# Kernel optimization log

Hardware: AMD Instinct MI355X
Metric: run time of the kernel (lower is better)

Reference implementation:

```python
import jax, jax.numpy as jnp
import numpy as np
import math

R, C, B, E, H, F = 64, 256, 1, 768, 12, 3072
D = E // H  # head dim = 64
EPS = 1e-6  # flax LayerNorm default


def _ln(x, s, b):
    mu = jnp.mean(x, axis=-1, keepdims=True)
    var = jnp.mean((x - mu) ** 2, axis=-1, keepdims=True)
    return (x - mu) * jax.lax.rsqrt(var + EPS) * s + b


def setup_inputs() -> dict:
    key = jax.random.key(0)
    ks = jax.random.split(key, 16)
    w = lambda k, sh: jax.random.normal(k, sh, jnp.float32) * 0.02
    z = lambda sh: jnp.zeros(sh, jnp.float32)
    return {
        "x": jax.random.normal(ks[0], (R, C, B, E), jnp.float32),
        "ln1_s": jnp.ones((E,), jnp.float32), "ln1_b": z((E,)),
        "r_wq": w(ks[1], (E, E)), "r_bq": z((E,)),
        "r_wk": w(ks[2], (E, E)), "r_bk": z((E,)),
        "r_wv": w(ks[3], (E, E)), "r_bv": z((E,)),
        "r_wo": w(ks[4], (E, E)), "r_bo": z((E,)),
        "ln2_s": jnp.ones((E,), jnp.float32), "ln2_b": z((E,)),
        "c_wq": w(ks[5], (E, E)), "c_bq": z((E,)),
        "c_wk": w(ks[6], (E, E)), "c_bk": z((E,)),
        "c_wv": w(ks[7], (E, E)), "c_bv": z((E,)),
        "c_wo": w(ks[8], (E, E)), "c_bo": z((E,)),
        "ln3_s": jnp.ones((E,), jnp.float32), "ln3_b": z((E,)),
        "f_w1": w(ks[9], (E, F)), "f_b1": z((F,)),
        "f_w2": w(ks[10], (F, E)), "f_b2": z((E,)),
    }


def reference(x, ln1_s, ln1_b, r_wq, r_bq, r_wk, r_bk, r_wv, r_bv, r_wo, r_bo,
              ln2_s, ln2_b, c_wq, c_bq, c_wk, c_bk, c_wv, c_bv, c_wo, c_bo,
              ln3_s, ln3_b, f_w1, f_b1, f_w2, f_b2):
    qkv = (R, C, B, H, D)
    # --- tied row self-attention (NOTE: original code has no residual adds) ---
    h = _ln(x, ln1_s, ln1_b)
    q = (h @ r_wq + r_bq).reshape(qkv) * (D ** -0.5 / math.sqrt(R))  # tied-row scaling
    k = (h @ r_wk + r_bk).reshape(qkv)
    v = (h @ r_wv + r_bv).reshape(qkv)
    aw = jnp.einsum('rinhd,rjnhd->hnij', q, k)  # single softmax tied across rows
    ap = jax.nn.softmax(aw, axis=-1)
    ctx = jnp.einsum('hnij,rjnhd->rinhd', ap, v).reshape(R, C, B, E)
    x = ctx @ r_wo + r_bo
    # --- column self-attention (per-column attention over rows) ---
    h = _ln(x, ln2_s, ln2_b)
    q = (h @ c_wq + c_bq).reshape(qkv) * (D ** -0.5)
    k = (h @ c_wk + c_bk).reshape(qkv)
    v = (h @ c_wv + c_bv).reshape(qkv)
    aw = jnp.einsum('icnhd,jcnhd->hcnij', q, k)
    ap = jax.nn.softmax(aw, axis=-1)
    ctx = jnp.einsum('hcnij,jcnhd->icnhd', ap, v).reshape(R, C, B, E)
    x = ctx @ c_wo + c_bo
    # --- FFN (gelu approximate=True matches flax default) ---
    h = _ln(x, ln3_s, ln3_b)
    return jax.nn.gelu(h @ f_w1 + f_b1) @ f_w2 + f_b2
```

## Files before the change

### kernel.cpp

```cpp
#include <hip/hip_runtime.h>
#include <hip/hip_bf16.h>
#include <stdint.h>
#include <stddef.h>

#define R_ 64
#define C_ 256
#define E_ 768
#define H_ 12
#define F_ 3072
#define D_ 64
#define NT_ (R_*C_)
#define HCRD_ ((size_t)H_*C_*R_*D_)

typedef float f32x4 __attribute__((ext_vector_type(4)));
typedef __bf16 bf16x8 __attribute__((ext_vector_type(8)));
typedef unsigned short us4 __attribute__((ext_vector_type(4)));
typedef unsigned short us8 __attribute__((ext_vector_type(8)));

typedef __attribute__((address_space(3))) uint32_t lds_u32;
typedef __attribute__((address_space(1))) uint32_t glb_u32;

__device__ __forceinline__ void gld16(const uint16_t* g, uint16_t* l) {
  __builtin_amdgcn_global_load_lds((const glb_u32*)g, (lds_u32*)l, 16, 0, 0);
}

__device__ __forceinline__ uint16_t f2b(float f) {
  __bf16 h = (__bf16)f;
  return *(uint16_t*)&h;
}

#define VM_WAIT6 { asm volatile("s_waitcnt vmcnt(6)" ::: "memory"); __builtin_amdgcn_sched_barrier(0); }
#define VM_WAIT4 { asm volatile("s_waitcnt vmcnt(4)" ::: "memory"); __builtin_amdgcn_sched_barrier(0); }
#define VM_WAIT0 { asm volatile("s_waitcnt vmcnt(0)" ::: "memory"); __builtin_amdgcn_sched_barrier(0); }
#define BARRIER  { __builtin_amdgcn_s_barrier(); __builtin_amdgcn_sched_barrier(0); }

enum { EP_F32B = 0, EP_GELU = 1, EP_AW = 2, EP_CTX = 3, EP_QKVROW = 4, EP_QKVCOL = 5 };

template<int EP, bool PERM>
__global__ __launch_bounds__(512, 2)
void gemm256(const uint16_t* __restrict__ A, const uint16_t* __restrict__ B,
             const float* __restrict__ bias, const float* __restrict__ biasK,
             const float* __restrict__ biasV, void* __restrict__ out,
             int N, int K, int lda, int ldb, float scale)
{
  __shared__ uint16_t lds[2][4][8192];
  const int tid  = threadIdx.x;
  const int wave = tid >> 6, lane = tid & 63;
  const int wm = wave >> 2, wn = wave & 3;
  const int lr = lane & 15, lq = lane >> 4;

  int lin = blockIdx.x + gridDim.x * blockIdx.y;
  const int q8 = (gridDim.x * gridDim.y) >> 3;
  const int wid = (lin & 7) * q8 + (lin >> 3);
  const int bx = wid % gridDim.x, by = wid / gridDim.x;
  const long bm = (long)by * 256, bn = (long)bx * 256;

  const int r0 = tid >> 2;
  const int csw = (((tid & 3) ^ ((r0 >> 1) & 3)) * 8);
  long am0 = bm + r0, am1 = bm + r0 + 128;
  if constexpr (PERM) {
    am0 = ((am0 & 63) << 8) | (am0 >> 6);
    am1 = ((am1 & 63) << 8) | (am1 >> 6);
  }
  const uint16_t* aR0 = A + am0 * (long)lda + csw;
  const uint16_t* aR1 = A + am1 * (long)lda + csw;
  const uint16_t* bR0 = B + (bn + r0) * (long)ldb + csw;
  const uint16_t* bR1 = B + (bn + r0 + 128) * (long)ldb + csw;

  auto stageH = [&](int s) {
    const int u = s >> 2, j = s & 3;
    const int kb = u * 64 + (j >> 1) * 32;
    uint16_t* d = &lds[u & 1][j][0];
    if (j & 1) { gld16(aR0 + kb, d + tid * 8); gld16(aR1 + kb, d + (tid + 512) * 8); }
    else       { gld16(bR0 + kb, d + tid * 8); gld16(bR1 + kb, d + (tid + 512) * 8); }
  };
  auto aoff = [&](int row) { return row * 32 + ((lq ^ ((row >> 1) & 3)) * 8); };

  f32x4 acc[8][4];
#pragma unroll
  for (int i = 0; i < 8; ++i)
#pragma unroll
    for (int j = 0; j < 4; ++j) acc[i][j] = (f32x4){0.f, 0.f, 0.f, 0.f};

  const int nt = K >> 6;
  stageH(0); stageH(1); stageH(2); stageH(3);
  VM_WAIT4;
  stageH(4); stageH(5); stageH(6);
  VM_WAIT6;
  BARRIER;

  for (int t = 0; t < nt; ++t) {
    const int buf = t & 1;
    const uint16_t* B0h = &lds[buf][0][0];
    const uint16_t* A0h = &lds[buf][1][0];
    const uint16_t* B1h = &lds[buf][2][0];
    const uint16_t* A1h = &lds[buf][3][0];
    const int s0 = 4 * t + 7;
    bf16x8 af[4], bf[4];

#pragma unroll
    for (int i = 0; i < 4; ++i) {
      bf[i] = *(const bf16x8*)&B0h[aoff(wn * 64 + i * 16 + lr)];
      af[i] = *(const bf16x8*)&A0h[aoff(wm * 128 + i * 16 + lr)];
    }
    if (s0 < 4 * nt) stageH(s0);
    BARRIER;
    __builtin_amdgcn_s_setprio(1);
#pragma unroll
    for (int mi = 0; mi < 4; ++mi)
#pragma unroll
      for (int ni = 0; ni < 4; ++ni)
        acc[mi][ni] = __builtin_amdgcn_mfma_f32_16x16x32_bf16(af[mi], bf[ni], acc[mi][ni], 0, 0, 0);
    __builtin_amdgcn_s_setprio(0);
    BARRIER;

#pragma unroll
    for (int i = 0; i < 4; ++i)
      af[i] = *(const bf16x8*)&A0h[aoff(wm * 128 + 64 + i * 16 + lr)];
    if (s0 + 1 < 4 * nt) stageH(s0 + 1);
    BARRIER;
    __builtin_amdgcn_s_setprio(1);
#pragma unroll
    for (int mi = 0; mi < 4; ++mi)
#pragma unroll
      for (int ni = 0; ni < 4; ++ni)
        acc[4 + mi][ni] = __builtin_amdgcn_mfma_f32_16x16x32_bf16(af[mi], bf[ni], acc[4 + mi][ni], 0, 0, 0);
    __builtin_amdgcn_s_setprio(0);
    BARRIER;

#pragma unroll
    for (int i = 0; i < 4; ++i) {
      bf[i] = *(const bf16x8*)&B1h[aoff(wn * 64 + i * 16 + lr)];
      af[i] = *(const bf16x8*)&A1h[aoff(wm * 128 + i * 16 + lr)];
    }
    if (s0 + 2 < 4 * nt) stageH(s0 + 2);
    BARRIER;
    __builtin_amdgcn_s_setprio(1);
#pragma unroll
    for (int mi = 0; mi < 4; ++mi)
#pragma unroll
      for (int ni = 0; ni < 4; ++ni)
        acc[mi][ni] = __builtin_amdgcn_mfma_f32_16x16x32_bf16(af[mi], bf[ni], acc[mi][ni], 0, 0, 0);
    __builtin_amdgcn_s_setprio(0);
    BARRIER;

#pragma unroll
    for (int i = 0; i < 4; ++i)
      af[i] = *(const bf16x8*)&A1h[aoff(wm * 128 + 64 + i * 16 + lr)];
    if (s0 + 3 < 4 * nt) stageH(s0 + 3);
    BARRIER;
    __builtin_amdgcn_s_setprio(1);
#pragma unroll
    for (int mi = 0; mi < 4; ++mi)
#pragma unroll
      for (int ni = 0; ni < 4; ++ni)
        acc[4 + mi][ni] = __builtin_amdgcn_mfma_f32_16x16x32_bf16(af[mi], bf[ni], acc[4 + mi][ni], 0, 0, 0);
    __builtin_amdgcn_s_setprio(0);
    if (t < nt - 2)       VM_WAIT6
    else if (t == nt - 2) VM_WAIT0
    BARRIER;
  }
  __syncthreads();

  if constexpr (EP == EP_F32B) {
#pragma unroll
    for (int mi = 0; mi < 8; ++mi)
#pragma unroll
      for (int ni = 0; ni < 4; ++ni)
#pragma unroll
        for (int r = 0; r < 4; ++r) {
          const long row = bm + wm * 128 + mi * 16 + lq * 4 + r;
          const long col = bn + wn * 64 + ni * 16 + lr;
          ((float*)out)[row * N + col] = acc[mi][ni][r] + bias[col];
        }
  } else {
    uint16_t* slabW = ((uint16_t*)lds) + (size_t)wave * 8192;
    const long colb = bn + wn * 64;
    int grp = 0; long cc0 = colb;
    const float* bb = bias;
    if constexpr (EP != EP_GELU) {
      grp = colb >= 1536 ? 2 : (colb >= 768 ? 1 : 0);
      cc0 = colb - (long)grp * 768;
      bb = grp == 0 ? bias : (grp == 1 ? biasK : biasV);
    }
    const bool tr = (EP != EP_GELU) && (grp == 2);
#pragma unroll
    for (int sub = 0; sub < 2; ++sub) {
      uint16_t* slab = slabW + sub * 4096;
      const long m0 = bm + wm * 128 + sub * 64;
#pragma unroll
      for (int mi = 0; mi < 4; ++mi)
#pragma unroll
        for (int ni = 0; ni < 4; ++ni)
#pragma unroll
          for (int r = 0; r < 4; ++r) {
            const int lrow = mi * 16 + lq * 4 + r;
            const int lcol = ni * 16 + lr;
            float val;
            if constexpr (EP == EP_GELU) {
              const float t = acc[sub * 4 + mi][ni][r] + bias[colb + lcol];
              const float u = 0.7978845608028654f * (t + 0.044715f * t * t * t);
              const float e = __expf(2.f * u);
              val = 0.5f * t * (2.f - 2.f / (e + 1.f));
            } else {
              val = acc[sub * 4 + mi][ni][r] + bb[cc0 + lcol];
              if (grp == 0) val *= scale;
            }
            const int sr = tr ? lcol : lrow;
            const int sc = tr ? lrow : lcol;
            const int psc = (sc & 7) | ((((sc >> 3) ^ (sr & 7))) << 3);
            slab[sr * 64 + psc] = f2b(val);
          }
      uint16_t* o16 = (uint16_t*)out;
      long obase, rstride;
      if constexpr (EP == EP_GELU) {
        obase = m0 * (long)N + colb; rstride = N;
      } else {
        const long h = cc0 >> 6;
        if constexpr (EP == EP_QKVROW) {
          const long rr = m0 >> 8, c0 = m0 & 255;
          if (grp < 2) { obase = (size_t)grp * HCRD_ + ((h * C_ + c0) * R_ + rr) * D_; rstride = R_ * D_; }
          else         { obase = 2 * HCRD_ + ((h * R_ + rr) * D_) * C_ + c0;           rstride = C_; }
        } else {
          const long cq = m0 >> 6;
          if (grp < 2) { obase = (size_t)grp * HCRD_ + ((h * C_ + cq) * R_) * D_; rstride = D_; }
          else         { obase = 2 * HCRD_ + ((h * C_ + cq) * D_) * R_;           rstride = R_; }
        }
      }
      const int rl = lane >> 3, chn = lane & 7;
#pragma unroll
      for (int pp = 0; pp < 8; ++pp) {
        const int srow = pp * 8 + rl;
        const int pch = chn ^ (srow & 7);
        us8 wv = *(const us8*)&slab[srow * 64 + pch * 8];
        *(us8*)(o16 + obase + (long)srow * rstride + chn * 8) = wv;
      }
    }
  }
}

template<int EP>
__global__ __launch_bounds__(256)
void gemm_bt(const uint16_t* __restrict__ A, const uint16_t* __restrict__ B,
             void* __restrict__ out,
             int M, int N, int K, int lda, int ldb, long sAz, long sBz)
{
  __shared__ uint16_t As[3][4096];
  __shared__ uint16_t Bs[3][4096];
  const int tid  = threadIdx.x;
  const int wave = tid >> 6, lane = tid & 63;
  const int z = blockIdx.z;

  const long bm = (long)blockIdx.y * 128;
  int kc = 0; long bnb = blockIdx.x;
  if constexpr (EP == EP_AW) { kc = blockIdx.x & 3; bnb = blockIdx.x >> 2; }
  const long bn = bnb * 128;
  const int wr = (wave >> 1) * 64;
  const int wc = (wave & 1) * 64;
  const int lr = lane & 15;
  const int lq = lane >> 4;

  const int t0 = tid, t1 = tid + 256;
  const int ar0 = t0 >> 2, ar1 = t1 >> 2;
  const int ac0 = (((t0 & 3) ^ ((ar0 >> 1) & 3)) * 8);
  const int ac1 = (((t1 & 3) ^ ((ar1 >> 1) & 3)) * 8);

  const uint16_t* a0p = A + (long)z * sAz + (bm + ar0) * (long)lda + (long)kc * 1024;
  const uint16_t* a1p = A + (long)z * sAz + (bm + ar1) * (long)lda + (long)kc * 1024;
  const uint16_t* b0p = B + (long)z * sBz + (bn + ar0) * (long)ldb + (long)kc * 1024;
  const uint16_t* b1p = B + (long)z * sBz + (bn + ar1) * (long)ldb + (long)kc * 1024;

  auto STAGE = [&](int bi, int kt) {
    gld16(a0p + kt + ac0, &As[bi][t0 * 8]);
    gld16(a1p + kt + ac1, &As[bi][t1 * 8]);
    gld16(b0p + kt + ac0, &Bs[bi][t0 * 8]);
    gld16(b1p + kt + ac1, &Bs[bi][t1 * 8]);
  };

  int apos[4], bpos[4];
#pragma unroll
  for (int i = 0; i < 4; ++i) {
    const int ra = wr + i * 16 + lr;
    const int rb = wc + i * 16 + lr;
    apos[i] = ra * 32 + (lq ^ ((ra >> 1) & 3)) * 8;
    bpos[i] = rb * 32 + (lq ^ ((rb >> 1) & 3)) * 8;
  }

  f32x4 acc[4][4];
#pragma unroll
  for (int i = 0; i < 4; ++i)
#pragma unroll
    for (int j = 0; j < 4; ++j) acc[i][j] = (f32x4){0.f, 0.f, 0.f, 0.f};

  const int nt = K >> 5;
  STAGE(0, 0);
  if (nt > 1) { STAGE(1, 32); VM_WAIT4; } else { VM_WAIT0; }
  BARRIER;

  int cur = 0;
  for (int t = 0; t < nt; ++t) {
    if (t + 2 < nt) {
      int sl = cur + 2; if (sl >= 3) sl -= 3;
      STAGE(sl, (t + 2) << 5);
    }
    bf16x8 af[4], bfm[4];
#pragma unroll
    for (int i = 0; i < 4; ++i) {
      af[i]  = *(const bf16x8*)&As[cur][apos[i]];
      bfm[i] = *(const bf16x8*)&Bs[cur][bpos[i]];
    }
    __builtin_amdgcn_s_setprio(1);
#pragma unroll
    for (int mi = 0; mi < 4; ++mi)
#pragma unroll
      for (int ni = 0; ni < 4; ++ni)
        acc[mi][ni] = __builtin_amdgcn_mfma_f32_16x16x32_bf16(af[mi], bfm[ni], acc[mi][ni], 0, 0, 0);
    __builtin_amdgcn_s_setprio(0);

    if (t + 2 < nt)      { VM_WAIT4; BARRIER; }
    else if (t + 1 < nt) { VM_WAIT0; BARRIER; }
    cur = (cur == 2) ? 0 : cur + 1;
  }

#pragma unroll
  for (int mi = 0; mi < 4; ++mi)
#pragma unroll
    for (int ni = 0; ni < 4; ++ni)
#pragma unroll
      for (int r = 0; r < 4; ++r) {
        const long row = bm + wr + mi * 16 + lq * 4 + r;
        const long col = bn + wc + ni * 16 + lr;
        if constexpr (EP == EP_AW) {
          ((float*)out)[((long)(z * 4 + kc) * M + row) * N + col] = acc[mi][ni][r];
        } else {
          ((uint16_t*)out)[((col >> 6) * C_ + row) * E_ + (long)z * 64 + (col & 63)] =
              f2b(acc[mi][ni][r]);
        }
      }
}

__global__ __launch_bounds__(256)
void ln_k(const float* __restrict__ x, const float* __restrict__ s, const float* __restrict__ b,
          uint16_t* __restrict__ out)
{
  const int wave = threadIdx.x >> 6, lane = threadIdx.x & 63;
  const long row = (long)blockIdx.x * 4 + wave;
  const float* xr = x + row * E_;
  f32x4 v[3];
  float sum = 0.f, sq = 0.f;
#pragma unroll
  for (int i = 0; i < 3; ++i) {
    v[i] = *(const f32x4*)(xr + (i * 64 + lane) * 4);
#pragma unroll
    for (int j = 0; j < 4; ++j) { sum += v[i][j]; sq += v[i][j] * v[i][j]; }
  }
#pragma unroll
  for (int m = 1; m < 64; m <<= 1) { sum += __shfl_xor(sum, m); sq += __shfl_xor(sq, m); }
  const float mu = sum * (1.f / E_);
  const float var = sq * (1.f / E_) - mu * mu;
  const float rs = rsqrtf(var + 1e-6f);
  uint16_t* orow = out + row * E_;
#pragma unroll
  for (int i = 0; i < 3; ++i) {
    const int e0 = (i * 64 + lane) * 4;
    us4 o;
#pragma unroll
    for (int j = 0; j < 4; ++j) o[j] = f2b((v[i][j] - mu) * rs * s[e0 + j] + b[e0 + j]);
    *(us4*)(orow + e0) = o;
  }
}

__global__ __launch_bounds__(256)
void softmax_k4(const float* __restrict__ aw4, uint16_t* __restrict__ ap)
{
  const int wave = threadIdx.x >> 6, lane = threadIdx.x & 63;
  const long row = (long)blockIdx.x * 4 + wave;
  const long h = row >> 8, i = row & 255;
  f32x4 v = (f32x4){0.f, 0.f, 0.f, 0.f};
#pragma unroll
  for (int kc = 0; kc < 4; ++kc) {
    f32x4 t = *(const f32x4*)(aw4 + (((h * 4 + kc) * C_ + i) * C_) + lane * 4);
#pragma unroll
    for (int j = 0; j < 4; ++j) v[j] += t[j];
  }
  float m = fmaxf(fmaxf(v[0], v[1]), fmaxf(v[2], v[3]));
#pragma unroll
  for (int k = 1; k < 64; k <<= 1) m = fmaxf(m, __shfl_xor(m, k));
  f32x4 e; float s = 0.f;
#pragma unroll
  for (int j = 0; j < 4; ++j) { e[j] = __expf(v[j] - m); s += e[j]; }
#pragma unroll
  for (int k = 1; k < 64; k <<= 1) s += __shfl_xor(s, k);
  const float inv = 1.f / s;
  us4 o;
#pragma unroll
  for (int j = 0; j < 4; ++j) o[j] = f2b(e[j] * inv);
  *(us4*)(ap + row * C_ + lane * 4) = o;
}

__global__ __launch_bounds__(256)
void tcvt(const float* __restrict__ in, uint16_t* __restrict__ out, int K, int N)
{
  __shared__ float t[32][33];
  const int tx = threadIdx.x, ty = threadIdx.y;
  const long k0 = (long)blockIdx.y * 32, n0 = (long)blockIdx.x * 32;
  for (int i = ty; i < 32; i += 8) t[i][tx] = in[(k0 + i) * N + n0 + tx];
  __syncthreads();
  for (int i = ty; i < 32; i += 8) out[(n0 + i) * K + k0 + tx] = f2b(t[tx][i]);
}

__global__ __launch_bounds__(64)
void colattn(const uint16_t* __restrict__ q, const uint16_t* __restrict__ k,
             const uint16_t* __restrict__ v, uint16_t* __restrict__ ctx)
{
  __shared__ uint16_t Qs[64 * 64];
  __shared__ uint16_t Ks[64 * 64];
  __shared__ uint16_t Vs[64 * 64];
  const int hc = blockIdx.x;
  const int h = hc >> 8, c = hc & 255;
  const int lane = threadIdx.x;
  const uint16_t* qb = q + (long)hc * (R_ * D_);
  const uint16_t* kb = k + (long)hc * (R_ * D_);
  const uint16_t* vb = v + (long)hc * (D_ * R_);
#pragma unroll
  for (int it = 0; it < 8; ++it) {
    const int o = (it * 64 + lane) * 8;
    gld16(qb + o, &Qs[o]);
    gld16(kb + o, &Ks[o]);
    gld16(vb + o, &Vs[o]);
  }
  asm volatile("s_waitcnt vmcnt(0)" ::: "memory");
  __builtin_amdgcn_sched_barrier(0);

  const int lr = lane & 15, lq = lane >> 4;
  f32x4 acc[4][4];
#pragma unroll
  for (int i = 0; i < 4; ++i)
#pragma unroll
    for (int j = 0; j < 4; ++j) acc[i][j] = (f32x4){0.f, 0.f, 0.f, 0.f};

#pragma unroll
  for (int kt = 0; kt < 2; ++kt) {
    bf16x8 af[4], bfm[4];
#pragma unroll
    for (int i = 0; i < 4; ++i) {
      af[i]  = *(const bf16x8*)&Qs[(i * 16 + lr) * 64 + kt * 32 + lq * 8];
      bfm[i] = *(const bf16x8*)&Ks[(i * 16 + lr) * 64 + kt * 32 + lq * 8];
    }
#pragma unroll
    for (int mi = 0; mi < 4; ++mi)
#pragma unroll
      for (int ni = 0; ni < 4; ++ni)
        acc[mi][ni] = __builtin_amdgcn_mfma_f32_16x16x32_bf16(af[mi], bfm[ni], acc[mi][ni], 0, 0, 0);
  }

#pragma unroll
  for (int mi = 0; mi < 4; ++mi) {
#pragma unroll
    for (int r = 0; r < 4; ++r) {
      float mx = fmaxf(fmaxf(acc[mi][0][r], acc[mi][1][r]), fmaxf(acc[mi][2][r], acc[mi][3][r]));
#pragma unroll
      for (int s = 1; s < 16; s <<= 1) mx = fmaxf(mx, __shfl_xor(mx, s));
      float e0 = __expf(acc[mi][0][r] - mx), e1 = __expf(acc[mi][1][r] - mx);
      float e2 = __expf(acc[mi][2][r] - mx), e3 = __expf(acc[mi][3][r] - mx);
      float sum = e0 + e1 + e2 + e3;
#pragma unroll
      for (int s = 1; s < 16; s <<= 1) sum += __shfl_xor(sum, s);
      const float inv = 1.f / sum;
      const int i = mi * 16 + lq * 4 + r;
      Qs[i * 64 +  0 + lr] = f2b(e0 * inv);
      Qs[i * 64 + 16 + lr] = f2b(e1 * inv);
      Qs[i * 64 + 32 + lr] = f2b(e2 * inv);
      Qs[i * 64 + 48 + lr] = f2b(e3 * inv);
    }
  }
  __syncthreads();

  f32x4 o_[4][4];
#pragma unroll
  for (int i = 0; i < 4; ++i)
#pragma unroll
    for (int j = 0; j < 4; ++j) o_[i][j] = (f32x4){0.f, 0.f, 0.f, 0.f};

#pragma unroll
  for (int kt = 0; kt < 2; ++kt) {
    bf16x8 pa[4], vv[4];
#pragma unroll
    for (int i = 0; i < 4; ++i) {
      pa[i] = *(const bf16x8*)&Qs[(i * 16 + lr) * 64 + kt * 32 + lq * 8];
      vv[i] = *(const bf16x8*)&Vs[(i * 16 + lr) * 64 + kt * 32 + lq * 8];
    }
#pragma unroll
    for (int mi = 0; mi < 4; ++mi)
#pragma unroll
      for (int ni = 0; ni < 4; ++ni)
        o_[mi][ni] = __builtin_amdgcn_mfma_f32_16x16x32_bf16(pa[mi], vv[ni], o_[mi][ni], 0, 0, 0);
  }

#pragma unroll
  for (int mi = 0; mi < 4; ++mi)
#pragma unroll
    for (int ni = 0; ni < 4; ++ni)
#pragma unroll
      for (int r = 0; r < 4; ++r) {
        const int i = mi * 16 + lq * 4 + r;
        const int d = ni * 16 + lr;
        ctx[((long)i * C_ + c) * E_ + h * 64 + d] = f2b(o_[mi][ni][r]);
      }
}

extern "C" void kernel_launch(void* const* d_in, const int* in_sizes, int n_in,
                              void* d_out, int out_size, void* d_ws, size_t ws_size,
                              hipStream_t stream)
{
  (void)in_sizes; (void)n_in; (void)out_size; (void)ws_size;
  const float* x     = (const float*)d_in[0];
  const float* ln1_s = (const float*)d_in[1];
  const float* ln1_b = (const float*)d_in[2];
  const float* r_wq  = (const float*)d_in[3];
  const float* r_bq  = (const float*)d_in[4];
  const float* r_wk  = (const float*)d_in[5];
  const float* r_bk  = (const float*)d_in[6];
  const float* r_wv  = (const float*)d_in[7];
  const float* r_bv  = (const float*)d_in[8];
  const float* r_wo  = (const float*)d_in[9];
  const float* r_bo  = (const float*)d_in[10];
  const float* ln2_s = (const float*)d_in[11];
  const float* ln2_b = (const float*)d_in[12];
  const float* c_wq  = (const float*)d_in[13];
  const float* c_bq  = (const float*)d_in[14];
  const float* c_wk  = (const float*)d_in[15];
  const float* c_bk  = (const float*)d_in[16];
  const float* c_wv  = (const float*)d_in[17];
  const float* c_bv  = (const float*)d_in[18];
  const float* c_wo  = (const float*)d_in[19];
  const float* c_bo  = (const float*)d_in[20];
  const float* ln3_s = (const float*)d_in[21];
  const float* ln3_b = (const float*)d_in[22];
  const float* f_w1  = (const float*)d_in[23];
  const float* f_b1  = (const float*)d_in[24];
  const float* f_w2  = (const float*)d_in[25];
  const float* f_b2  = (const float*)d_in[26];

  uint8_t* p = (uint8_t*)d_ws;
  auto take = [&p](size_t n) { uint8_t* r = p; p += (n + 255) & ~(size_t)255; return r; };

  uint16_t* wqkv1 = (uint16_t*)take((size_t)3 * E_ * E_ * 2);
  uint16_t* wqkv2 = (uint16_t*)take((size_t)3 * E_ * E_ * 2);
  uint16_t* rwoT  = (uint16_t*)take((size_t)E_ * E_ * 2);
  uint16_t* cwoT  = (uint16_t*)take((size_t)E_ * E_ * 2);
  uint16_t* w1T   = (uint16_t*)take((size_t)E_ * F_ * 2);
  uint16_t* w2T   = (uint16_t*)take((size_t)F_ * E_ * 2);
  uint16_t* hb    = (uint16_t*)take((size_t)NT_ * E_ * 2);
  uint16_t* qkvT  = (uint16_t*)take(3 * HCRD_ * 2);
  uint16_t* qT = qkvT, *kT = qkvT + HCRD_, *vT = qkvT + 2 * HCRD_;
  uint16_t* ctxb  = (uint16_t*)take((size_t)NT_ * E_ * 2);
  uint16_t* apb   = (uint16_t*)take((size_t)H_ * C_ * C_ * 2);
  uint16_t* g     = qkvT;
  float*    awb4  = (float*)ctxb;
  float*    x1    = (float*)d_out;

  const dim3 tb32(32, 8);
  const dim3 gEE(E_ / 32, E_ / 32);
  tcvt<<<gEE, tb32, 0, stream>>>(r_wq, wqkv1 + 0 * E_ * E_, E_, E_);
  tcvt<<<gEE, tb32, 0, stream>>>(r_wk, wqkv1 + 1 * E_ * E_, E_, E_);
  tcvt<<<gEE, tb32, 0, stream>>>(r_wv, wqkv1 + 2 * E_ * E_, E_, E_);
  tcvt<<<gEE, tb32, 0, stream>>>(c_wq, wqkv2 + 0 * E_ * E_, E_, E_);
  tcvt<<<gEE, tb32, 0, stream>>>(c_wk, wqkv2 + 1 * E_ * E_, E_, E_);
  tcvt<<<gEE, tb32, 0, stream>>>(c_wv, wqkv2 + 2 * E_ * E_, E_, E_);
  tcvt<<<gEE, tb32, 0, stream>>>(r_wo, rwoT, E_, E_);
  tcvt<<<gEE, tb32, 0, stream>>>(c_wo, cwoT, E_, E_);
  tcvt<<<dim3(F_ / 32, E_ / 32), tb32, 0, stream>>>(f_w1, w1T, E_, F_);
  tcvt<<<dim3(E_ / 32, F_ / 32), tb32, 0, stream>>>(f_w2, w2T, F_, E_);

  ln_k<<<NT_ / 4, 256, 0, stream>>>(x, ln1_s, ln1_b, hb);
  gemm256<EP_QKVROW, false><<<dim3(9, 64), 512, 0, stream>>>(
      hb, wqkv1, r_bq, r_bk, r_bv, qkvT, 3 * E_, E_, E_, E_, 0.015625f);
  gemm_bt<EP_AW><<<dim3(8, 2, H_), 256, 0, stream>>>(
      qT, kT, awb4, C_, C_, 1024, R_ * D_, R_ * D_, (long)C_ * R_ * D_, (long)C_ * R_ * D_);
  softmax_k4<<<(H_ * C_) / 4, 256, 0, stream>>>(awb4, apb);
  gemm_bt<EP_CTX><<<dim3((R_ * D_) / 128, 2, H_), 256, 0, stream>>>(
      apb, vT, ctxb, C_, R_ * D_, C_, C_, C_, (long)C_ * C_, (long)R_ * D_ * C_);
  gemm256<EP_F32B, false><<<dim3(3, 64), 512, 0, stream>>>(
      ctxb, rwoT, r_bo, nullptr, nullptr, x1, E_, E_, E_, E_, 1.f);

  ln_k<<<NT_ / 4, 256, 0, stream>>>(x1, ln2_s, ln2_b, hb);
  gemm256<EP_QKVCOL, true><<<dim3(9, 64), 512, 0, stream>>>(
      hb, wqkv2, c_bq, c_bk, c_bv, qkvT, 3 * E_, E_, E_, E_, 0.125f);
  colattn<<<H_ * C_, 64, 0, stream>>>(qT, kT, vT, ctxb);
  gemm256<EP_F32B, false><<<dim3(3, 64), 512, 0, stream>>>(
      ctxb, cwoT, c_bo, nullptr, nullptr, x1, E_, E_, E_, E_, 1.f);

  ln_k<<<NT_ / 4, 256, 0, stream>>>(x1, ln3_s, ln3_b, hb);
  gemm256<EP_GELU, false><<<dim3(12, 64), 512, 0, stream>>>(
      hb, w1T, f_b1, nullptr, nullptr, g, F_, E_, E_, E_, 1.f);
  gemm256<EP_F32B, false><<<dim3(3, 64), 512, 0, stream>>>(
      g, w2T, f_b2, nullptr, nullptr, d_out, E_, F_, F_, F_, 1.f);
}
```

Baseline: 574.2 us.

## Simplify GEMM pipelines to plain double buffering with full-tile syncs

Replaces the fine-grained 8-stage half-tile pipeline in the 256x256 GEMM with a simple double buffer: the whole 64-wide K tile is loaded at once, all MFMAs run, then the kernel waits for all loads and barriers. The 128x128 batched GEMM drops from a 3-slot ring with prefetch depth 2 to a 2-slot double buffer. This cuts barrier count and register pressure but shortens how far loads run ahead of compute, so memory latency is hidden less well. The wider LDS layout uses an 8-way XOR swizzle.

```diff
diff --git a/kernel.cpp b/kernel.cpp
--- a/kernel.cpp
+++ b/kernel.cpp
@@ -29,10 +29,10 @@
   return *(uint16_t*)&h;
 }
 
-#define VM_WAIT6 { asm volatile("s_waitcnt vmcnt(6)" ::: "memory"); __builtin_amdgcn_sched_barrier(0); }
-#define VM_WAIT4 { asm volatile("s_waitcnt vmcnt(4)" ::: "memory"); __builtin_amdgcn_sched_barrier(0); }
-#define VM_WAIT0 { asm volatile("s_waitcnt vmcnt(0)" ::: "memory"); __builtin_amdgcn_sched_barrier(0); }
-#define BARRIER  { __builtin_amdgcn_s_barrier(); __builtin_amdgcn_sched_barrier(0); }
+#define TILE_SYNC { asm volatile("s_waitcnt vmcnt(0)" ::: "memory"); \
+                    __builtin_amdgcn_s_barrier(); \
+                    __builtin_amdgcn_sched_barrier(0); }
+#define BAR_ONLY  { __builtin_amdgcn_s_barrier(); __builtin_amdgcn_sched_barrier(0); }
 
 enum { EP_F32B = 0, EP_GELU = 1, EP_AW = 2, EP_CTX = 3, EP_QKVROW = 4, EP_QKVCOL = 5 };
 
@@ -43,7 +43,8 @@
              const float* __restrict__ biasV, void* __restrict__ out,
              int N, int K, int lda, int ldb, float scale)
 {
-  __shared__ uint16_t lds[2][4][8192];
+  __shared__ uint16_t As2[2][16384];
+  __shared__ uint16_t Bs2[2][16384];
   const int tid  = threadIdx.x;
   const int wave = tid >> 6, lane = tid & 63;
   const int wm = wave >> 2, wn = wave & 3;
@@ -55,26 +56,27 @@
   const int bx = wid % gridDim.x, by = wid / gridDim.x;
   const long bm = (long)by * 256, bn = (long)bx * 256;
 
-  const int r0 = tid >> 2;
-  const int csw = (((tid & 3) ^ ((r0 >> 1) & 3)) * 8);
-  long am0 = bm + r0, am1 = bm + r0 + 128;
-  if constexpr (PERM) {
-    am0 = ((am0 & 63) << 8) | (am0 >> 6);
-    am1 = ((am1 & 63) << 8) | (am1 >> 6);
-  }
-  const uint16_t* aR0 = A + am0 * (long)lda + csw;
-  const uint16_t* aR1 = A + am1 * (long)lda + csw;
-  const uint16_t* bR0 = B + (bn + r0) * (long)ldb + csw;
-  const uint16_t* bR1 = B + (bn + r0 + 128) * (long)ldb + csw;
-
-  auto stageH = [&](int s) {
-    const int u = s >> 2, j = s & 3;
-    const int kb = u * 64 + (j >> 1) * 32;
-    uint16_t* d = &lds[u & 1][j][0];
-    if (j & 1) { gld16(aR0 + kb, d + tid * 8); gld16(aR1 + kb, d + (tid + 512) * 8); }
-    else       { gld16(bR0 + kb, d + tid * 8); gld16(bR1 + kb, d + (tid + 512) * 8); }
+  const int r0 = tid >> 3;
+  const int c8 = (((tid & 7) ^ (r0 & 7)) << 3);
+  const uint16_t* aSrc[4];
+  const uint16_t* bSrc[4];
+#pragma unroll
+  for (int i = 0; i < 4; ++i) {
+    long am = bm + r0 + 64 * i;
+    if constexpr (PERM) am = ((am & 63) << 8) | (am >> 6);
+    aSrc[i] = A + am * (long)lda + c8;
+    bSrc[i] = B + (bn + r0 + 64 * i) * (long)ldb + c8;
+  }
+
+  auto stage = [&](int u) {
+    const int b = u & 1;
+    const int kb = u << 6;
+#pragma unroll
+    for (int i = 0; i < 4; ++i) gld16(aSrc[i] + kb, &As2[b][tid * 8 + 4096 * i]);
+#pragma unroll
+    for (int i = 0; i < 4; ++i) gld16(bSrc[i] + kb, &Bs2[b][tid * 8 + 4096 * i]);
   };
-  auto aoff = [&](int row) { return row * 32 + ((lq ^ ((row >> 1) & 3)) * 8); };
+  auto rdoff = [&](int row, int c) { return row * 64 + (((c ^ (row & 7))) << 3); };
 
   f32x4 acc[8][4];
 #pragma unroll
@@ -83,82 +85,29 @@
     for (int j = 0; j < 4; ++j) acc[i][j] = (f32x4){0.f, 0.f, 0.f, 0.f};
 
   const int nt = K >> 6;
-  stageH(0); stageH(1); stageH(2); stageH(3);
-  VM_WAIT4;
-  stageH(4); stageH(5); stageH(6);
-  VM_WAIT6;
-  BARRIER;
+  stage(0);
+  TILE_SYNC;
 
   for (int t = 0; t < nt; ++t) {
-    const int buf = t & 1;
-    const uint16_t* B0h = &lds[buf][0][0];
-    const uint16_t* A0h = &lds[buf][1][0];
-    const uint16_t* B1h = &lds[buf][2][0];
-    const uint16_t* A1h = &lds[buf][3][0];
-    const int s0 = 4 * t + 7;
-    bf16x8 af[4], bf[4];
-
-#pragma unroll
-    for (int i = 0; i < 4; ++i) {
-      bf[i] = *(const bf16x8*)&B0h[aoff(wn * 64 + i * 16 + lr)];
-      af[i] = *(const bf16x8*)&A0h[aoff(wm * 128 + i * 16 + lr)];
-    }
-    if (s0 < 4 * nt) stageH(s0);
-    BARRIER;
-    __builtin_amdgcn_s_setprio(1);
-#pragma unroll
-    for (int mi = 0; mi < 4; ++mi)
-#pragma unroll
-      for (int ni = 0; ni < 4; ++ni)
-        acc[mi][ni] = __builtin_amdgcn_mfma_f32_16x16x32_bf16(af[mi], bf[ni], acc[mi][ni], 0, 0, 0);
-    __builtin_amdgcn_s_setprio(0);
-    BARRIER;
-
-#pragma unroll
-    for (int i = 0; i < 4; ++i)
-      af[i] = *(const bf16x8*)&A0h[aoff(wm * 128 + 64 + i * 16 + lr)];
-    if (s0 + 1 < 4 * nt) stageH(s0 + 1);
-    BARRIER;
-    __builtin_amdgcn_s_setprio(1);
-#pragma unroll
-    for (int mi = 0; mi < 4; ++mi)
-#pragma unroll
-      for (int ni = 0; ni < 4; ++ni)
-        acc[4 + mi][ni] = __builtin_amdgcn_mfma_f32_16x16x32_bf16(af[mi], bf[ni], acc[4 + mi][ni], 0, 0, 0);
-    __builtin_amdgcn_s_setprio(0);
-    BARRIER;
-
-#pragma unroll
-    for (int i = 0; i < 4; ++i) {
-      bf[i] = *(const bf16x8*)&B1h[aoff(wn * 64 + i * 16 + lr)];
-      af[i] = *(const bf16x8*)&A1h[aoff(wm * 128 + i * 16 + lr)];
-    }
-    if (s0 + 2 < 4 * nt) stageH(s0 + 2);
-    BARRIER;
-    __builtin_amdgcn_s_setprio(1);
-#pragma unroll
-    for (int mi = 0; mi < 4; ++mi)
-#pragma unroll
-      for (int ni = 0; ni < 4; ++ni)
-        acc[mi][ni] = __builtin_amdgcn_mfma_f32_16x16x32_bf16(af[mi], bf[ni], acc[mi][ni], 0, 0, 0);
-    __builtin_amdgcn_s_setprio(0);
-    BARRIER;
-
-#pragma unroll
-    for (int i = 0; i < 4; ++i)
-      af[i] = *(const bf16x8*)&A1h[aoff(wm * 128 + 64 + i * 16 + lr)];
-    if (s0 + 3 < 4 * nt) stageH(s0 + 3);
-    BARRIER;
-    __builtin_amdgcn_s_setprio(1);
-#pragma unroll
-    for (int mi = 0; mi < 4; ++mi)
-#pragma unroll
-      for (int ni = 0; ni < 4; ++ni)
-        acc[4 + mi][ni] = __builtin_amdgcn_mfma_f32_16x16x32_bf16(af[mi], bf[ni], acc[4 + mi][ni], 0, 0, 0);
-    __builtin_amdgcn_s_setprio(0);
-    if (t < nt - 2)       VM_WAIT6
-    else if (t == nt - 2) VM_WAIT0
-    BARRIER;
+    const int b = t & 1;
+    if (t + 1 < nt) stage(t + 1);
+#pragma unroll
+    for (int kh = 0; kh < 2; ++kh) {
+      const int c = kh * 4 + lq;
+      bf16x8 bfr[4], afr[8];
+#pragma unroll
+      for (int i = 0; i < 4; ++i) bfr[i] = *(const bf16x8*)&Bs2[b][rdoff(wn * 64 + i * 16 + lr, c)];
+#pragma unroll
+      for (int i = 0; i < 8; ++i) afr[i] = *(const bf16x8*)&As2[b][rdoff(wm * 128 + i * 16 + lr, c)];
+      __builtin_amdgcn_s_setprio(1);
+#pragma unroll
+      for (int mi = 0; mi < 8; ++mi)
+#pragma unroll
+        for (int ni = 0; ni < 4; ++ni)
+          acc[mi][ni] = __builtin_amdgcn_mfma_f32_16x16x32_bf16(afr[mi], bfr[ni], acc[mi][ni], 0, 0, 0);
+      __builtin_amdgcn_s_setprio(0);
+    }
+    if (t + 1 < nt) { TILE_SYNC; } else { BAR_ONLY; }
   }
   __syncthreads();
 
@@ -174,7 +123,7 @@
           ((float*)out)[row * N + col] = acc[mi][ni][r] + bias[col];
         }
   } else {
-    uint16_t* slabW = ((uint16_t*)lds) + (size_t)wave * 8192;
+    uint16_t* slabW = (wave < 4) ? &As2[0][wave * 8192] : &Bs2[0][(wave - 4) * 8192];
     const long colb = bn + wn * 64;
     int grp = 0; long cc0 = colb;
     const float* bb = bias;
@@ -245,8 +194,8 @@
              void* __restrict__ out,
              int M, int N, int K, int lda, int ldb, long sAz, long sBz)
 {
-  __shared__ uint16_t As[3][4096];
-  __shared__ uint16_t Bs[3][4096];
+  __shared__ uint16_t As[2][4096];
+  __shared__ uint16_t Bs[2][4096];
   const int tid  = threadIdx.x;
   const int wave = tid >> 6, lane = tid & 63;
   const int z = blockIdx.z;
@@ -294,20 +243,16 @@
 
   const int nt = K >> 5;
   STAGE(0, 0);
-  if (nt > 1) { STAGE(1, 32); VM_WAIT4; } else { VM_WAIT0; }
-  BARRIER;
-
-  int cur = 0;
+  TILE_SYNC;
+
   for (int t = 0; t < nt; ++t) {
-    if (t + 2 < nt) {
-      int sl = cur + 2; if (sl >= 3) sl -= 3;
-      STAGE(sl, (t + 2) << 5);
-    }
+    const int b = t & 1;
+    if (t + 1 < nt) STAGE(b ^ 1, (t + 1) << 5);
     bf16x8 af[4], bfm[4];
 #pragma unroll
     for (int i = 0; i < 4; ++i) {
-      af[i]  = *(const bf16x8*)&As[cur][apos[i]];
-      bfm[i] = *(const bf16x8*)&Bs[cur][bpos[i]];
+      af[i]  = *(const bf16x8*)&As[b][apos[i]];
+      bfm[i] = *(const bf16x8*)&Bs[b][bpos[i]];
     }
     __builtin_amdgcn_s_setprio(1);
 #pragma unroll
@@ -316,10 +261,7 @@
       for (int ni = 0; ni < 4; ++ni)
         acc[mi][ni] = __builtin_amdgcn_mfma_f32_16x16x32_bf16(af[mi], bfm[ni], acc[mi][ni], 0, 0, 0);
     __builtin_amdgcn_s_setprio(0);
-
-    if (t + 2 < nt)      { VM_WAIT4; BARRIER; }
-    else if (t + 1 < nt) { VM_WAIT0; BARRIER; }
-    cur = (cur == 2) ? 0 : cur + 1;
+    if (t + 1 < nt) { TILE_SYNC; }
   }
 
 #pragma unroll
```

New measurement: 596.6 us. 3.9% more time.
